# Kernel tuning notes

Hardware: AMD Instinct MI355X
Metric: run time of the kernel (lower is better)

Reference implementation:

```python
import jax, jax.numpy as jnp
import numpy as np


def setup_inputs() -> dict:
    key = jax.random.key(0)
    B, D, C, H = 4096, 64, 128, 512
    ks = jax.random.split(key, 6)
    return {
        "q_z_x_params": jax.random.normal(ks[0], (B, C), jnp.float32),
        "eps": jax.random.normal(ks[1], (B, D), jnp.float32),
        "W1": jax.random.normal(ks[2], (D + C, H), jnp.float32) / np.sqrt(D + C).astype(np.float32),
        "b1": jnp.zeros((H,), jnp.float32),
        "W2": jax.random.normal(ks[3], (H, H), jnp.float32) / np.sqrt(H).astype(np.float32),
        "b2": jnp.zeros((H,), jnp.float32),
        "W3": jax.random.normal(ks[4], (H, 2 * D), jnp.float32) / np.sqrt(H).astype(np.float32),
        "b3": jnp.zeros((2 * D,), jnp.float32),
    }


def _made_masks(D, C, H):
    # Standard MADE degrees, natural ordering; context columns fully connected.
    m_in = np.arange(1, D + 1)                      # input degrees 1..D
    m_h = (np.arange(H) % (D - 1)) + 1              # hidden degrees 1..D-1
    M1 = np.concatenate([m_h[None, :] >= m_in[:, None],
                         np.ones((C, H), bool)], axis=0)   # (D+C, H)
    M2 = m_h[None, :] >= m_h[:, None]               # (H, H)
    m_out = np.tile(np.arange(1, D + 1), 2)         # (2D,) mean||prescale
    M3 = m_out[None, :] > m_h[:, None]              # (H, 2D)
    f32 = jnp.float32
    return jnp.asarray(M1, f32), jnp.asarray(M2, f32), jnp.asarray(M3, f32)


def reference(q_z_x_params, eps, W1, b1, W2, b2, W3, b3):
    B, D = eps.shape
    C = q_z_x_params.shape[1]
    H = W2.shape[0]
    M1, M2, M3 = _made_masks(D, C, H)
    mW1, mW2, mW3 = W1 * M1, W2 * M2, W3 * M3

    def made(z):
        x = jnp.concatenate([z, q_z_x_params], axis=1)   # (B, D+C)
        h1 = jax.nn.relu(x @ mW1 + b1)
        h2 = jax.nn.relu(h1 @ mW2 + b2)
        out = h2 @ mW3 + b3                              # (B, 2D)
        return out[:, :D], out[:, D:]

    def step(z, i):
        mean, prescale = made(z)
        mu_i = jnp.take(mean, i, axis=1)                 # (B,)
        scale_i = jax.nn.softplus(jnp.take(prescale, i, axis=1))
        z_i = mu_i + scale_i * jnp.take(eps, i, axis=1)  # reparameterized Normal sample
        z = z.at[:, i].set(z_i)
        return z, None

    z0 = jnp.zeros((B, D), eps.dtype)
    z_sample, _ = jax.lax.scan(step, z0, jnp.arange(D))
    return z_sample
```

## Files before the change

kernel.cpp:

```cpp
#include <hip/hip_runtime.h>
#include <math.h>

#define DD 64
#define CC 128
#define HH 512
#define BATCH 4096

__global__ void transpose_w3(const float* __restrict__ W3, float* __restrict__ W3T) {
    int idx = blockIdx.x * blockDim.x + threadIdx.x;
    int c = idx >> 9;
    int j = idx & 511;
    W3T[idx] = W3[j * (2 * DD) + c];
}

__device__ __forceinline__ float fast_softplus(float x) {
    float t = exp2f(-fabsf(x) * 1.44269504f);
    return fmaxf(x, 0.f) + 0.69314718f * log2f(1.f + t);
}

__device__ __forceinline__ float bcast(float x, int l) {
    return __int_as_float(__builtin_amdgcn_readlane(__float_as_int(x), l));
}

#define DPP_ADD(x, ctrl, rm)                                                          \
    x += __int_as_float(__builtin_amdgcn_update_dpp(0, __float_as_int(x), ctrl, rm, 0xf, true))
__device__ __forceinline__ float wave_allsum(float x) {
    DPP_ADD(x, 0x111, 0xf);
    DPP_ADD(x, 0x112, 0xf);
    DPP_ADD(x, 0x114, 0xf);
    DPP_ADD(x, 0x118, 0xf);
    DPP_ADD(x, 0x142, 0xa);
    DPP_ADD(x, 0x143, 0xc);
    return bcast(x, 63);
}

typedef const __attribute__((address_space(1))) void* as1_cptr;
typedef __attribute__((address_space(3))) void* as3_ptr;
__device__ __forceinline__ void glds16(const float* g, float* l) {
    __builtin_amdgcn_global_load_lds((as1_cptr)g, (as3_ptr)l, 16, 0, 0);
}

__global__ __launch_bounds__(256, 2) void made_sample(
    const float* __restrict__ ctx,
    const float* __restrict__ eps,
    const float* __restrict__ W1,
    const float* __restrict__ b1,
    const float* __restrict__ W2,
    const float* __restrict__ b2,
    const float* __restrict__ b3,
    const float* __restrict__ W3T,
    float* __restrict__ out)
{
    const int lane  = threadIdx.x & 63;
    const int w     = threadIdx.x >> 6;
    const int rbase = blockIdx.x * 8 + w * 2;
    const int jbase = 8 * lane;

    __shared__ float sbuf[2][12 * HH];

    int deg[8];
    #pragma unroll
    for (int u = 0; u < 8; ++u) deg[u] = (jbase + u) % 63 + 1;

    auto load8lds = [&](const float* base, float* r) {
        float4 a = *(const float4*)(base + lane * 4);
        float4 b = *(const float4*)(base + 256 + lane * 4);
        r[0] = a.x; r[1] = a.y; r[2] = a.z; r[3] = a.w;
        r[4] = b.x; r[5] = b.y; r[6] = b.z; r[7] = b.w;
    };
    auto stage_row = [&](const float* src, float* dst) {
        glds16(src + lane * 8,     dst);
        glds16(src + lane * 8 + 4, dst + 256);
    };

    float p1[2][8], p2[2][8], h2[2][8];
    {
        #pragma unroll
        for (int u = 0; u < 8; ++u) {
            float t1 = b1[jbase + u];
            float t2 = b2[jbase + u];
            p1[0][u] = t1; p1[1][u] = t1;
            p2[0][u] = t2; p2[1][u] = t2;
            h2[0][u] = 0.f; h2[1][u] = 0.f;
        }
    }

    float ca[2], cb[2], ep[2];
    #pragma unroll
    for (int r = 0; r < 2; ++r) {
        ca[r] = ctx[(rbase + r) * CC + lane];
        cb[r] = ctx[(rbase + r) * CC + 64 + lane];
        ep[r] = eps[(rbase + r) * DD + lane];
    }
    const float b3m = b3[lane];
    const float b3p = b3[64 + lane];

    auto stage_ctx = [&](int ch, float* buf) {
        #pragma unroll
        for (int q2 = 0; q2 < 2; ++q2) {
            const int q = 2 * w + q2;
            stage_row(W1 + (DD + 8 * ch + q) * HH, buf + q * HH);
        }
    };
    auto stage_step = [&](int in, float* buf) {
        const int basen = (in == 0) ? 0 : (in - 1);
        #pragma unroll
        for (int rr = 0; rr < 3; ++rr) {
            const int r = w + 4 * rr;
            const float* src;
            if (r < 9) {
                int k = basen + 63 * r;
                if (k >= HH) k = HH - 8;
                src = W2 + k * HH;
            } else if (r == 9) {
                src = W3T + in * HH;
            } else if (r == 10) {
                src = W3T + (DD + in) * HH;
            } else {
                src = W1 + in * HH;
            }
            stage_row(src, buf + r * HH);
        }
    };

    stage_ctx(0, sbuf[0]);
    __syncthreads();
    #pragma unroll 1
    for (int ch = 0; ch < 16; ++ch) {
        float* cur = sbuf[ch & 1];
        float* nxt = sbuf[(ch + 1) & 1];
        if (ch < 15) stage_ctx(ch + 1, nxt);
        else         stage_step(0, sbuf[0]);
        #pragma unroll
        for (int q = 0; q < 8; ++q) {
            float wv[8];
            load8lds(cur + q * HH, wv);
            const int c = 8 * ch + q;
            #pragma unroll
            for (int r = 0; r < 2; ++r) {
                const float srcv = (ch < 8) ? ca[r] : cb[r];
                const float cv = bcast(srcv, c & 63);
                #pragma unroll
                for (int u = 0; u < 8; ++u) p1[r][u] = fmaf(cv, wv[u], p1[r][u]);
            }
        }
        __syncthreads();
    }

    float z[2] = {0.f, 0.f};

    #pragma unroll 1
    for (int i = 0; i < DD; ++i) {
        float* cur = sbuf[i & 1];
        float* nxt = sbuf[(i + 1) & 1];
        if (i < 63) stage_step(i + 1, nxt);

        float wm[8], wp[8], w1r[8];
        load8lds(cur + 9 * HH, wm);
        load8lds(cur + 10 * HH, wp);
        load8lds(cur + 11 * HH, w1r);

        float m[2];
        #pragma unroll
        for (int r = 0; r < 2; ++r) {
            float mv = 0.f;
            #pragma unroll
            for (int u = 0; u < 8; ++u) mv = (deg[u] == i) ? p1[r][u] : mv;
            m[r] = fmaxf(mv, 0.f);
        }

        const int base = (i == 0) ? 0 : (i - 1);
        #pragma unroll
        for (int t = 0; t < 9; ++t) {
            const int k = base + 63 * t;
            float wv[8];
            load8lds(cur + t * HH, wv);
            float ha[2];
            if (t == 8) {
                const float vm = (k < HH) ? 1.f : 0.f;
                #pragma unroll
                for (int r = 0; r < 2; ++r) ha[r] = vm * bcast(m[r], 63);
            } else {
                #pragma unroll
                for (int r = 0; r < 2; ++r) ha[r] = bcast(m[r], k >> 3);
            }
            #pragma unroll
            for (int u = 0; u < 8; ++u)
                #pragma unroll
                for (int r = 0; r < 2; ++r) p2[r][u] = fmaf(ha[r], wv[u], p2[r][u]);
        }

        #pragma unroll
        for (int r = 0; r < 2; ++r)
            #pragma unroll
            for (int u = 0; u < 8; ++u)
                if (deg[u] == i) h2[r][u] = fmaxf(p2[r][u], 0.f);

        float macc[2], qacc[2];
        #pragma unroll
        for (int r = 0; r < 2; ++r) {
            float ma = 0.f, qa = 0.f;
            #pragma unroll
            for (int u = 0; u < 8; ++u) {
                ma = fmaf(h2[r][u], wm[u], ma);
                qa = fmaf(h2[r][u], wp[u], qa);
            }
            macc[r] = ma; qacc[r] = qa;
        }
        const float bm = bcast(b3m, i);
        const float bp = bcast(b3p, i);
        #pragma unroll
        for (int r = 0; r < 2; ++r) {
            const float mt = wave_allsum(macc[r]) + bm;
            const float qt = wave_allsum(qacc[r]) + bp;
            const float sp = fast_softplus(qt);
            const float ei = bcast(ep[r], i);
            const float zi = fmaf(sp, ei, mt);
            if (lane == i) z[r] = zi;
            #pragma unroll
            for (int u = 0; u < 8; ++u) p1[r][u] = fmaf(zi, w1r[u], p1[r][u]);
        }

        __syncthreads();
    }

    #pragma unroll
    for (int r = 0; r < 2; ++r) out[(rbase + r) * DD + lane] = z[r];
}

extern "C" void kernel_launch(void* const* d_in, const int* in_sizes, int n_in,
                              void* d_out, int out_size, void* d_ws, size_t ws_size,
                              hipStream_t stream) {
    const float* ctx = (const float*)d_in[0];
    const float* eps = (const float*)d_in[1];
    const float* W1  = (const float*)d_in[2];
    const float* b1  = (const float*)d_in[3];
    const float* W2  = (const float*)d_in[4];
    const float* b2  = (const float*)d_in[5];
    const float* W3  = (const float*)d_in[6];
    const float* b3  = (const float*)d_in[7];
    float* W3T = (float*)d_ws;

    transpose_w3<<<(2 * DD * HH) / 256, 256, 0, stream>>>(W3, W3T);
    made_sample<<<BATCH / 8, 256, 0, stream>>>(ctx, eps, W1, b1, W2, b2, b3, W3T,
                                               (float*)d_out);
}
```

Measured before the change: 191.2 us.

## Accumulate output layer incrementally per step, drop W3 transpose and wave reductions

```diff
diff --git a/kernel.cpp b/kernel.cpp
--- a/kernel.cpp
+++ b/kernel.cpp
@@ -6,12 +6,9 @@
 #define HH 512
 #define BATCH 4096
 
-__global__ void transpose_w3(const float* __restrict__ W3, float* __restrict__ W3T) {
-    int idx = blockIdx.x * blockDim.x + threadIdx.x;
-    int c = idx >> 9;
-    int j = idx & 511;
-    W3T[idx] = W3[j * (2 * DD) + c];
-}
+typedef __attribute__((ext_vector_type(2))) float f32x2;
+
+__device__ __forceinline__ f32x2 splat2(float x) { f32x2 v; v[0] = x; v[1] = x; return v; }
 
 __device__ __forceinline__ float fast_softplus(float x) {
     float t = exp2f(-fabsf(x) * 1.44269504f);
@@ -20,18 +17,6 @@
 
 __device__ __forceinline__ float bcast(float x, int l) {
     return __int_as_float(__builtin_amdgcn_readlane(__float_as_int(x), l));
-}
-
-#define DPP_ADD(x, ctrl, rm)                                                          \
-    x += __int_as_float(__builtin_amdgcn_update_dpp(0, __float_as_int(x), ctrl, rm, 0xf, true))
-__device__ __forceinline__ float wave_allsum(float x) {
-    DPP_ADD(x, 0x111, 0xf);
-    DPP_ADD(x, 0x112, 0xf);
-    DPP_ADD(x, 0x114, 0xf);
-    DPP_ADD(x, 0x118, 0xf);
-    DPP_ADD(x, 0x142, 0xa);
-    DPP_ADD(x, 0x143, 0xc);
-    return bcast(x, 63);
 }
 
 typedef const __attribute__((address_space(1))) void* as1_cptr;
@@ -47,8 +32,8 @@
     const float* __restrict__ b1,
     const float* __restrict__ W2,
     const float* __restrict__ b2,
+    const float* __restrict__ W3,
     const float* __restrict__ b3,
-    const float* __restrict__ W3T,
     float* __restrict__ out)
 {
     const int lane  = threadIdx.x & 63;
@@ -56,34 +41,34 @@
     const int rbase = blockIdx.x * 8 + w * 2;
     const int jbase = 8 * lane;
 
-    __shared__ float sbuf[2][12 * HH];
+    __shared__ float sbuf[2][10 * HH];
 
     int deg[8];
     #pragma unroll
     for (int u = 0; u < 8; ++u) deg[u] = (jbase + u) % 63 + 1;
 
-    auto load8lds = [&](const float* base, float* r) {
-        float4 a = *(const float4*)(base + lane * 4);
-        float4 b = *(const float4*)(base + 256 + lane * 4);
-        r[0] = a.x; r[1] = a.y; r[2] = a.z; r[3] = a.w;
-        r[4] = b.x; r[5] = b.y; r[6] = b.z; r[7] = b.w;
+    auto load8v = [&](const float* base_, f32x2* r_) {
+        float4 a = *(const float4*)(base_ + lane * 4);
+        float4 b = *(const float4*)(base_ + 256 + lane * 4);
+        r_[0][0] = a.x; r_[0][1] = a.y; r_[1][0] = a.z; r_[1][1] = a.w;
+        r_[2][0] = b.x; r_[2][1] = b.y; r_[3][0] = b.z; r_[3][1] = b.w;
     };
     auto stage_row = [&](const float* src, float* dst) {
         glds16(src + lane * 8,     dst);
         glds16(src + lane * 8 + 4, dst + 256);
     };
 
-    float p1[2][8], p2[2][8], h2[2][8];
-    {
-        #pragma unroll
-        for (int u = 0; u < 8; ++u) {
-            float t1 = b1[jbase + u];
-            float t2 = b2[jbase + u];
-            p1[0][u] = t1; p1[1][u] = t1;
-            p2[0][u] = t2; p2[1][u] = t2;
-            h2[0][u] = 0.f; h2[1][u] = 0.f;
-        }
-    }
+    f32x2 p1[2][4], p2[2][4], acc[2];
+    #pragma unroll
+    for (int j = 0; j < 4; ++j) {
+        f32x2 t1, t2;
+        t1[0] = b1[jbase + 2 * j]; t1[1] = b1[jbase + 2 * j + 1];
+        t2[0] = b2[jbase + 2 * j]; t2[1] = b2[jbase + 2 * j + 1];
+        p1[0][j] = t1; p1[1][j] = t1;
+        p2[0][j] = t2; p2[1][j] = t2;
+    }
+    acc[0] = splat2(0.f);
+    acc[1] = splat2(0.f);
 
     float ca[2], cb[2], ep[2];
     #pragma unroll
@@ -107,19 +92,17 @@
         #pragma unroll
         for (int rr = 0; rr < 3; ++rr) {
             const int r = w + 4 * rr;
-            const float* src;
-            if (r < 9) {
-                int k = basen + 63 * r;
-                if (k >= HH) k = HH - 8;
-                src = W2 + k * HH;
-            } else if (r == 9) {
-                src = W3T + in * HH;
-            } else if (r == 10) {
-                src = W3T + (DD + in) * HH;
-            } else {
-                src = W1 + in * HH;
-            }
-            stage_row(src, buf + r * HH);
+            if (r <= 9) {
+                const float* src;
+                if (r < 9) {
+                    int k = basen + 63 * r;
+                    if (k >= HH) k = HH - 8;
+                    src = W2 + k * HH;
+                } else {
+                    src = W1 + in * HH;
+                }
+                stage_row(src, buf + r * HH);
+            }
         }
     };
 
@@ -133,15 +116,15 @@
         else         stage_step(0, sbuf[0]);
         #pragma unroll
         for (int q = 0; q < 8; ++q) {
-            float wv[8];
-            load8lds(cur + q * HH, wv);
+            f32x2 wv[4];
+            load8v(cur + q * HH, wv);
             const int c = 8 * ch + q;
             #pragma unroll
             for (int r = 0; r < 2; ++r) {
-                const float srcv = (ch < 8) ? ca[r] : cb[r];
-                const float cv = bcast(srcv, c & 63);
+                const float cv = bcast((ch < 8) ? ca[r] : cb[r], c & 63);
+                const f32x2 cv2 = splat2(cv);
                 #pragma unroll
-                for (int u = 0; u < 8; ++u) p1[r][u] = fmaf(cv, wv[u], p1[r][u]);
+                for (int j = 0; j < 4; ++j) p1[r][j] += cv2 * wv[j];
             }
         }
         __syncthreads();
@@ -155,70 +138,88 @@
         float* nxt = sbuf[(i + 1) & 1];
         if (i < 63) stage_step(i + 1, nxt);
 
-        float wm[8], wp[8], w1r[8];
-        load8lds(cur + 9 * HH, wm);
-        load8lds(cur + 10 * HH, wp);
-        load8lds(cur + 11 * HH, w1r);
+        const int base = (i == 0) ? 0 : (i - 1);
+
+        f32x2 w3v[9];
+        #pragma unroll
+        for (int t = 0; t < 9; ++t) {
+            const int k  = base + 63 * t;
+            const int ks = (k < HH) ? k : (HH - 1);
+            w3v[t][0] = W3[ks * (2 * DD) + lane];
+            w3v[t][1] = W3[ks * (2 * DD) + 64 + lane];
+        }
 
         float m[2];
         #pragma unroll
         for (int r = 0; r < 2; ++r) {
             float mv = 0.f;
             #pragma unroll
-            for (int u = 0; u < 8; ++u) mv = (deg[u] == i) ? p1[r][u] : mv;
+            for (int u = 0; u < 8; ++u)
+                mv = (deg[u] == i) ? p1[r][u >> 1][u & 1] : mv;
             m[r] = fmaxf(mv, 0.f);
         }
 
-        const int base = (i == 0) ? 0 : (i - 1);
         #pragma unroll
         for (int t = 0; t < 9; ++t) {
             const int k = base + 63 * t;
-            float wv[8];
-            load8lds(cur + t * HH, wv);
-            float ha[2];
+            f32x2 wv[4];
+            load8v(cur + t * HH, wv);
+            float h0, h1v;
             if (t == 8) {
                 const float vm = (k < HH) ? 1.f : 0.f;
-                #pragma unroll
-                for (int r = 0; r < 2; ++r) ha[r] = vm * bcast(m[r], 63);
+                h0  = vm * bcast(m[0], 63);
+                h1v = vm * bcast(m[1], 63);
             } else {
-                #pragma unroll
-                for (int r = 0; r < 2; ++r) ha[r] = bcast(m[r], k >> 3);
-            }
+                h0  = bcast(m[0], k >> 3);
+                h1v = bcast(m[1], k >> 3);
+            }
+            const f32x2 h0v = splat2(h0), h1vv = splat2(h1v);
+            #pragma unroll
+            for (int j = 0; j < 4; ++j) {
+                p2[0][j] += h0v  * wv[j];
+                p2[1][j] += h1vv * wv[j];
+            }
+        }
+
+        float hn[2];
+        #pragma unroll
+        for (int r = 0; r < 2; ++r) {
+            float hv = 0.f;
             #pragma unroll
             for (int u = 0; u < 8; ++u)
-                #pragma unroll
-                for (int r = 0; r < 2; ++r) p2[r][u] = fmaf(ha[r], wv[u], p2[r][u]);
-        }
-
-        #pragma unroll
-        for (int r = 0; r < 2; ++r)
-            #pragma unroll
-            for (int u = 0; u < 8; ++u)
-                if (deg[u] == i) h2[r][u] = fmaxf(p2[r][u], 0.f);
-
-        float macc[2], qacc[2];
+                hv = (deg[u] == i) ? p2[r][u >> 1][u & 1] : hv;
+            hn[r] = fmaxf(hv, 0.f);
+        }
+
+        #pragma unroll
+        for (int t = 0; t < 9; ++t) {
+            const int k = base + 63 * t;
+            float h0, h1v;
+            if (t == 8) {
+                const float vm = (k < HH) ? 1.f : 0.f;
+                h0  = vm * bcast(hn[0], 63);
+                h1v = vm * bcast(hn[1], 63);
+            } else {
+                h0  = bcast(hn[0], k >> 3);
+                h1v = bcast(hn[1], k >> 3);
+            }
+            acc[0] += splat2(h0)  * w3v[t];
+            acc[1] += splat2(h1v) * w3v[t];
+        }
+
+        f32x2 w1v[4];
+        load8v(cur + 9 * HH, w1v);
         #pragma unroll
         for (int r = 0; r < 2; ++r) {
-            float ma = 0.f, qa = 0.f;
-            #pragma unroll
-            for (int u = 0; u < 8; ++u) {
-                ma = fmaf(h2[r][u], wm[u], ma);
-                qa = fmaf(h2[r][u], wp[u], qa);
-            }
-            macc[r] = ma; qacc[r] = qa;
-        }
-        const float bm = bcast(b3m, i);
-        const float bp = bcast(b3p, i);
-        #pragma unroll
-        for (int r = 0; r < 2; ++r) {
-            const float mt = wave_allsum(macc[r]) + bm;
-            const float qt = wave_allsum(qacc[r]) + bp;
-            const float sp = fast_softplus(qt);
-            const float ei = bcast(ep[r], i);
-            const float zi = fmaf(sp, ei, mt);
+            const float am = acc[r][0] + b3m;
+            const float ap = acc[r][1] + b3p;
+            const float sp = fast_softplus(ap);
+            const float zc = fmaf(sp, ep[r], am);
+            const float zi = bcast(zc, i);
             if (lane == i) z[r] = zi;
-            #pragma unroll
-            for (int u = 0; u < 8; ++u) p1[r][u] = fmaf(zi, w1r[u], p1[r][u]);
+            const f32x2 zi2 = splat2(zi);
+            #pragma unroll
+            for (int j = 0; j < 4; ++j) p1[r][j] += zi2 * w1v[j];
         }
 
         __syncthreads();
@@ -239,9 +240,8 @@
     const float* b2  = (const float*)d_in[5];
     const float* W3  = (const float*)d_in[6];
     const float* b3  = (const float*)d_in[7];
-    float* W3T = (float*)d_ws;
-
-    transpose_w3<<<(2 * DD * HH) / 256, 256, 0, stream>>>(W3, W3T);
-    made_sample<<<BATCH / 8, 256, 0, stream>>>(ctx, eps, W1, b1, W2, b2, b3, W3T,
+    (void)d_ws; (void)ws_size; (void)in_sizes; (void)n_in; (void)out_size;
+
+    made_sample<<<BATCH / 8, 256, 0, stream>>>(ctx, eps, W1, b1, W2, b2, W3, b3,
                                                (float*)d_out);
 }
```

Measured after the change: 184.7 us. 1.04x faster.
